# Performance work log

Measured on AMD Instinct MI355X. Metric: run time of the kernel, lower is better.

The kernel has to match this reference:

```python
import jax, jax.numpy as jnp
import numpy as np

NUM_HEADS = 32
HEAD_SIZE = 128
NUM_KV_HEADS = 8
SCALE = 0.08838834764831845  # 1/sqrt(128)
SLIDING_WINDOW = 1024
B, S = 2, 2048


def setup_inputs() -> dict:
    key = jax.random.key(0)
    kq, kk, kv = jax.random.split(key, 3)
    query = jax.random.normal(kq, (B, S, NUM_HEADS * HEAD_SIZE), dtype=jnp.float32)
    k = jax.random.normal(kk, (B, S, NUM_KV_HEADS * HEAD_SIZE), dtype=jnp.float32)
    v = jax.random.normal(kv, (B, S, NUM_KV_HEADS * HEAD_SIZE), dtype=jnp.float32)
    return {"query": query, "key": k, "value": v}


def _attn(query, key, value):
    # [B, S, H, D] / [B, S, KVH, D]
    q = query.reshape(B, S, NUM_HEADS, HEAD_SIZE)
    k = key.reshape(B, S, NUM_KV_HEADS, HEAD_SIZE)
    v = value.reshape(B, S, NUM_KV_HEADS, HEAD_SIZE)
    group = NUM_HEADS // NUM_KV_HEADS
    # GQA: broadcast each kv head across its query-head group
    k = jnp.repeat(k, group, axis=2)  # [B, S, H, D]
    v = jnp.repeat(v, group, axis=2)
    scores = jnp.einsum('bqhd,bkhd->bhqk', q, k) * SCALE  # [B, H, S, S]
    qi = jnp.arange(S)[:, None]
    ki = jnp.arange(S)[None, :]
    # causal + sliding window: key at most SLIDING_WINDOW-1 behind query
    mask = (ki <= qi) & (qi - ki < SLIDING_WINDOW)  # [S, S]
    neg_inf = jnp.finfo(scores.dtype).min
    scores = jnp.where(mask[None, None], scores, neg_inf)
    probs = jax.nn.softmax(scores, axis=-1)
    out = jnp.einsum('bhqk,bkhd->bqhd', probs, v)
    return out.reshape(B, S, NUM_HEADS * HEAD_SIZE)


def reference(query, key, value):
    return _attn(query, key, value)
```

## Files before the change

kernel.cpp:

```cpp
#include <hip/hip_runtime.h>
#include <hip/hip_bf16.h>


#define H_Q 32
#define H_KV 8
#define HDIM 128
#define SEQLEN 2048
#define NBATCH 2
#define WIN 1024
#define QK_SCALE 0.08838834764831845f
#define LOG2E 1.4426950408889634f
#define SCALE_LOG2E (QK_SCALE * LOG2E)

#define NEG_BIG  (-3.0e38f)
#define NEG_CLMP (-1.0e30f)

#define QPITCH (H_Q * HDIM)
#define KPITCH (H_KV * HDIM)

typedef __attribute__((ext_vector_type(8))) short  short8;
typedef __attribute__((ext_vector_type(4))) short  short4v;
typedef __attribute__((ext_vector_type(4))) float  floatx4;

static __device__ __forceinline__ short bf16bits(float x) {
    return __builtin_bit_cast(short, __float2bfloat16(x));
}

#define TR_READ(dst, addr, OFFSTR) \
    asm volatile("ds_read_b64_tr_b16 %0, %1 offset:" OFFSTR : "=v"(dst) : "v"(addr))

#define CAT8(a, b) __builtin_shufflevector(a, b, 0, 1, 2, 3, 4, 5, 6, 7)

#define MFMA_BF16 __builtin_amdgcn_mfma_f32_16x16x32_bf16

__global__ __launch_bounds__(256, 2)
void fa_fwd(const float* __restrict__ Q,
            const float* __restrict__ K,
            const float* __restrict__ V,
            float* __restrict__ O)
{
    __shared__ __align__(16) short lds_k[64][136];
    __shared__ __align__(16) short lds_v[8][64][16];
    __shared__ __align__(16) short lds_pt[4][64][16];

    const int bi  = blockIdx.x;
    const int qt  = bi & 31;
    const int h   = (bi >> 5) & 31;
    const int b   = bi >> 10;
    const int kvh = h >> 2;
    const int q0  = qt << 6;

    const int tid  = threadIdx.x;
    const int wid  = tid >> 6;
    const int lane = tid & 63;
    const int ln16 = lane & 15;
    const int lg   = lane >> 4;

    const float* Qb = Q + (size_t)b * SEQLEN * QPITCH + (size_t)h * HDIM;
    const float* Kb = K + (size_t)b * SEQLEN * KPITCH + (size_t)kvh * HDIM;
    const float* Vb = V + (size_t)b * SEQLEN * KPITCH + (size_t)kvh * HDIM;
    float*       Ob = O + (size_t)b * SEQLEN * QPITCH + (size_t)h * HDIM;

    const uint32_t v_base  = (uint32_t)(uintptr_t)&lds_v[0][0][0]
                           + (uint32_t)(lg * 256 + ln16 * 8);
    const uint32_t pt_base = (uint32_t)(uintptr_t)&lds_pt[wid][0][0]
                           + (uint32_t)(lg * 256 + ln16 * 8);

    int kvlo = q0 - (WIN - 1);
    if (kvlo < 0) kvlo = 0;
    kvlo &= ~63;

    floatx4 pk[8], pv[8];
    auto issue_kv = [&](int kt) {
        #pragma unroll
        for (int i = 0; i < 8; ++i) {
            const int fi  = i * 256 + tid;
            const int key = fi >> 5;
            const int c4  = (fi & 31) * 4;
            const size_t grow = (size_t)(kt + key) * KPITCH + c4;
            pk[i] = *(const floatx4*)(Kb + grow);
            pv[i] = *(const floatx4*)(Vb + grow);
        }
    };
    issue_kv(kvlo);

    short8 qf[4];
    {
        const int qrow = q0 + wid * 16 + ln16;
        const float* qs = Qb + (size_t)qrow * QPITCH + lg * 8;
        #pragma unroll
        for (int kk = 0; kk < 4; ++kk) {
            floatx4 a = *(const floatx4*)(qs + kk * 32);
            floatx4 c = *(const floatx4*)(qs + kk * 32 + 4);
            short8 f;
            #pragma unroll
            for (int j = 0; j < 4; ++j) { f[j] = bf16bits(a[j]); f[4 + j] = bf16bits(c[j]); }
            qf[kk] = f;
        }
    }

    floatx4 oacc[8];
    #pragma unroll
    for (int i = 0; i < 8; ++i) oacc[i] = (floatx4){0.f, 0.f, 0.f, 0.f};
    float m_r[4], l_r[4];
    #pragma unroll
    for (int r = 0; r < 4; ++r) { m_r[r] = NEG_BIG; l_r[r] = 0.f; }

    for (int kk0 = kvlo; kk0 <= q0; kk0 += 64) {
        __syncthreads();
        #pragma unroll
        for (int i = 0; i < 8; ++i) {
            const int fi  = i * 256 + tid;
            const int key = fi >> 5;
            const int c4  = (fi & 31) * 4;
            short4v ksv, vsv;
            #pragma unroll
            for (int j = 0; j < 4; ++j) {
                ksv[j] = bf16bits(pk[i][j]);
                vsv[j] = bf16bits(pv[i][j]);
            }
            *(short4v*)&lds_k[key][c4] = ksv;
            *(short4v*)&lds_v[c4 >> 4][key][c4 & 15] = vsv;
        }
        __syncthreads();

        if (kk0 + 64 <= q0) issue_kv(kk0 + 64);

        float sc[4][4];
        #pragma unroll
        for (int nt = 0; nt < 4; ++nt) {
            floatx4 acc = (floatx4){0.f, 0.f, 0.f, 0.f};
            #pragma unroll
            for (int kk = 0; kk < 4; ++kk) {
                short8 kf = *(const short8*)&lds_k[nt * 16 + ln16][kk * 32 + lg * 8];
                acc = MFMA_BF16(qf[kk], kf, acc, 0, 0, 0);
            }
            #pragma unroll
            for (int r = 0; r < 4; ++r) sc[nt][r] = acc[r];
        }

        const bool full = (kk0 + 63 <= q0) && (kk0 >= q0 - 960);
        float pm[4];
        #pragma unroll
        for (int r = 0; r < 4; ++r) pm[r] = NEG_BIG;
        if (full) {
            #pragma unroll
            for (int nt = 0; nt < 4; ++nt)
                #pragma unroll
                for (int r = 0; r < 4; ++r) {
                    sc[nt][r] *= SCALE_LOG2E;
                    pm[r] = fmaxf(pm[r], sc[nt][r]);
                }
        } else {
            #pragma unroll
            for (int nt = 0; nt < 4; ++nt) {
                const int kcol = kk0 + nt * 16 + ln16;
                #pragma unroll
                for (int r = 0; r < 4; ++r) {
                    const int qrow = q0 + wid * 16 + lg * 4 + r;
                    const bool ok = (kcol <= qrow) && (qrow - kcol < WIN);
                    sc[nt][r] = ok ? sc[nt][r] * SCALE_LOG2E : NEG_BIG;
                    pm[r] = fmaxf(pm[r], sc[nt][r]);
                }
            }
        }
        #pragma unroll
        for (int r = 0; r < 4; ++r)
            #pragma unroll
            for (int off = 1; off < 16; off <<= 1)
                pm[r] = fmaxf(pm[r], __shfl_xor(pm[r], off, 16));

        float alpha[4], mne[4];
        #pragma unroll
        for (int r = 0; r < 4; ++r) {
            const float mn = fmaxf(m_r[r], pm[r]);
            const float me = fmaxf(mn, NEG_CLMP);
            alpha[r] = exp2f(m_r[r] - me);
            m_r[r] = mn;
            mne[r] = me;
        }

        float psum[4] = {0.f, 0.f, 0.f, 0.f};
        #pragma unroll
        for (int nt = 0; nt < 4; ++nt) {
            short4v pq;
            #pragma unroll
            for (int r = 0; r < 4; ++r) {
                const float p = exp2f(sc[nt][r] - mne[r]);
                psum[r] += p;
                pq[r] = bf16bits(p);
            }
            *(short4v*)&lds_pt[wid][nt * 16 + ln16][lg * 4] = pq;
        }
        #pragma unroll
        for (int r = 0; r < 4; ++r) {
            #pragma unroll
            for (int off = 1; off < 16; off <<= 1)
                psum[r] += __shfl_xor(psum[r], off, 16);
            l_r[r] = l_r[r] * alpha[r] + psum[r];
        }
        #pragma unroll
        for (int dt = 0; dt < 8; ++dt)
            #pragma unroll
            for (int r = 0; r < 4; ++r) oacc[dt][r] *= alpha[r];

        asm volatile("s_waitcnt lgkmcnt(0)" ::: "memory");
        __builtin_amdgcn_sched_barrier(0);

        #pragma unroll
        for (int ks = 0; ks < 2; ++ks) {
            const uint32_t pa = pt_base + (uint32_t)(ks * 1024);
            const uint32_t va = v_base  + (uint32_t)(ks * 1024);
            short4v p0, p1, w0a, w0b, w1a, w1b, w2a, w2b, w3a, w3b;
            TR_READ(p0,  pa, "0");     TR_READ(p1,  pa, "128");
            TR_READ(w0a, va, "0");     TR_READ(w0b, va, "128");
            TR_READ(w1a, va, "2048");  TR_READ(w1b, va, "2176");
            TR_READ(w2a, va, "4096");  TR_READ(w2b, va, "4224");
            TR_READ(w3a, va, "6144");  TR_READ(w3b, va, "6272");
            asm volatile("s_waitcnt lgkmcnt(0)" ::: "memory");
            __builtin_amdgcn_sched_barrier(0);
            const short8 pf = CAT8(p0, p1);
            oacc[0] = MFMA_BF16(pf, CAT8(w0a, w0b), oacc[0], 0, 0, 0);
            oacc[1] = MFMA_BF16(pf, CAT8(w1a, w1b), oacc[1], 0, 0, 0);
            oacc[2] = MFMA_BF16(pf, CAT8(w2a, w2b), oacc[2], 0, 0, 0);
            oacc[3] = MFMA_BF16(pf, CAT8(w3a, w3b), oacc[3], 0, 0, 0);
            short4v x0a, x0b, x1a, x1b, x2a, x2b, x3a, x3b;
            TR_READ(x0a, va, "8192");  TR_READ(x0b, va, "8320");
            TR_READ(x1a, va, "10240"); TR_READ(x1b, va, "10368");
            TR_READ(x2a, va, "12288"); TR_READ(x2b, va, "12416");
            TR_READ(x3a, va, "14336"); TR_READ(x3b, va, "14464");
            asm volatile("s_waitcnt lgkmcnt(0)" ::: "memory");
            __builtin_amdgcn_sched_barrier(0);
            oacc[4] = MFMA_BF16(pf, CAT8(x0a, x0b), oacc[4], 0, 0, 0);
            oacc[5] = MFMA_BF16(pf, CAT8(x1a, x1b), oacc[5], 0, 0, 0);
            oacc[6] = MFMA_BF16(pf, CAT8(x2a, x2b), oacc[6], 0, 0, 0);
            oacc[7] = MFMA_BF16(pf, CAT8(x3a, x3b), oacc[7], 0, 0, 0);
        }
    }

    #pragma unroll
    for (int r = 0; r < 4; ++r) {
        const float inv = 1.0f / l_r[r];
        const int qrow = q0 + wid * 16 + lg * 4 + r;
        float* dst = Ob + (size_t)qrow * QPITCH;
        #pragma unroll
        for (int dt = 0; dt < 8; ++dt)
            dst[dt * 16 + ln16] = oacc[dt][r] * inv;
    }
}

extern "C" void kernel_launch(void* const* d_in, const int* in_sizes, int n_in,
                              void* d_out, int out_size, void* d_ws, size_t ws_size,
                              hipStream_t stream) {
    const float* Q = (const float*)d_in[0];
    const float* K = (const float*)d_in[1];
    const float* V = (const float*)d_in[2];
    float* O = (float*)d_out;
    dim3 grid(NBATCH * H_Q * (SEQLEN / 64));
    fa_fwd<<<grid, 256, 0, stream>>>(Q, K, V, O);
}
```

Baseline: 341.2 us.

## Pre-convert K/V to bf16 tiled workspace and stage via direct global-to-LDS loads

```diff
diff --git a/kernel.cpp b/kernel.cpp
--- a/kernel.cpp
+++ b/kernel.cpp
@@ -18,6 +18,9 @@
 #define QPITCH (H_Q * HDIM)
 #define KPITCH (H_KV * HDIM)
 
+#define WS_ELEMS ((size_t)NBATCH * H_KV * SEQLEN * HDIM)
+#define WS_BYTES (2 * WS_ELEMS * sizeof(short))
+
 typedef __attribute__((ext_vector_type(8))) short  short8;
 typedef __attribute__((ext_vector_type(4))) short  short4v;
 typedef __attribute__((ext_vector_type(4))) float  floatx4;
@@ -30,21 +33,54 @@
     asm volatile("ds_read_b64_tr_b16 %0, %1 offset:" OFFSTR : "=v"(dst) : "v"(addr))
 
 #define CAT8(a, b) __builtin_shufflevector(a, b, 0, 1, 2, 3, 4, 5, 6, 7)
-
 #define MFMA_BF16 __builtin_amdgcn_mfma_f32_16x16x32_bf16
 
-__global__ __launch_bounds__(256, 2)
+#define GLOAD_LDS16(gp, loff)                                                   \
+    __builtin_amdgcn_global_load_lds(                                           \
+        (const __attribute__((address_space(1))) unsigned int*)(const void*)(gp), \
+        (__attribute__((address_space(3))) unsigned int*)(uintptr_t)(loff),     \
+        16, 0, 0)
+
+#define CVT_THREADS (WS_ELEMS / 4)
+#define CVT_BLOCKS  (CVT_THREADS / 256)
+
+__global__ __launch_bounds__(256)
+void cvt_kv(const float* __restrict__ K, const float* __restrict__ V,
+            short* __restrict__ wsK, short* __restrict__ wsV)
+{
+    const int idx = blockIdx.x * 256 + threadIdx.x;
+    if (idx >= (int)CVT_THREADS) return;
+    const int g   = idx & 31;
+    const int kvh = (idx >> 5) & 7;
+    const int s   = (idx >> 8) & 2047;
+    const int b   = idx >> 19;
+    const int d   = g * 4;
+
+    const size_t soff = ((size_t)(b * SEQLEN + s)) * KPITCH + kvh * HDIM + d;
+    floatx4 kk = *(const floatx4*)(K + soff);
+    floatx4 vv = *(const floatx4*)(V + soff);
+    short4v ks, vs;
+    #pragma unroll
+    for (int j = 0; j < 4; ++j) { ks[j] = bf16bits(kk[j]); vs[j] = bf16bits(vv[j]); }
+
+    const size_t tbase = (((size_t)(b * H_KV + kvh)) * 32 + (s >> 6)) * 8192;
+    *(short4v*)&wsK[tbase + (size_t)(s & 63) * 128 + (d ^ ((s & 7) << 3))] = ks;
+    *(short4v*)&wsV[tbase + (size_t)(d >> 4) * 1024 + (s & 63) * 16 + (d & 15)] = vs;
+}
+
+__global__ __launch_bounds__(256, 4)
 void fa_fwd(const float* __restrict__ Q,
-            const float* __restrict__ K,
-            const float* __restrict__ V,
+            const short* __restrict__ wsK,
+            const short* __restrict__ wsV,
             float* __restrict__ O)
 {
-    __shared__ __align__(16) short lds_k[64][136];
+    __shared__ __align__(16) short lds_k[64][128];
     __shared__ __align__(16) short lds_v[8][64][16];
     __shared__ __align__(16) short lds_pt[4][64][16];
 
-    const int bi  = blockIdx.x;
-    const int qt  = bi & 31;
+    int bi = blockIdx.x;
+    bi = (bi & 7) * 256 + (bi >> 3);
+    const int qt  = 31 - (bi & 31);
     const int h   = (bi >> 5) & 31;
     const int b   = bi >> 10;
     const int kvh = h >> 2;
@@ -55,14 +91,18 @@
     const int lane = tid & 63;
     const int ln16 = lane & 15;
     const int lg   = lane >> 4;
+    const int kxor = (ln16 & 7) << 3;
 
     const float* Qb = Q + (size_t)b * SEQLEN * QPITCH + (size_t)h * HDIM;
-    const float* Kb = K + (size_t)b * SEQLEN * KPITCH + (size_t)kvh * HDIM;
-    const float* Vb = V + (size_t)b * SEQLEN * KPITCH + (size_t)kvh * HDIM;
     float*       Ob = O + (size_t)b * SEQLEN * QPITCH + (size_t)h * HDIM;
-
-    const uint32_t v_base  = (uint32_t)(uintptr_t)&lds_v[0][0][0]
-                           + (uint32_t)(lg * 256 + ln16 * 8);
+    const char*  wsKh = (const char*)(wsK + ((size_t)(b * H_KV + kvh)) * (SEQLEN * HDIM));
+    const char*  wsVh = (const char*)(wsV + ((size_t)(b * H_KV + kvh)) * (SEQLEN * HDIM));
+
+    const uint32_t k_lds = (uint32_t)(uintptr_t)&lds_k[0][0];
+    const uint32_t v_lds = (uint32_t)(uintptr_t)&lds_v[0][0][0];
+    const uint32_t wave_off = (uint32_t)((tid & 0xC0) * 16);
+
+    const uint32_t v_base  = v_lds + (uint32_t)(lg * 256 + ln16 * 8);
     const uint32_t pt_base = (uint32_t)(uintptr_t)&lds_pt[wid][0][0]
                            + (uint32_t)(lg * 256 + ln16 * 8);
 
@@ -70,19 +110,21 @@
     if (kvlo < 0) kvlo = 0;
     kvlo &= ~63;
 
-    floatx4 pk[8], pv[8];
-    auto issue_kv = [&](int kt) {
-        #pragma unroll
-        for (int i = 0; i < 8; ++i) {
-            const int fi  = i * 256 + tid;
-            const int key = fi >> 5;
-            const int c4  = (fi & 31) * 4;
-            const size_t grow = (size_t)(kt + key) * KPITCH + c4;
-            pk[i] = *(const floatx4*)(Kb + grow);
-            pv[i] = *(const floatx4*)(Vb + grow);
-        }
+    auto stage_k = [&](int kt) {
+        const char* src = wsKh + (size_t)kt * 16384;
+        #pragma unroll
+        for (int i = 0; i < 4; ++i)
+            GLOAD_LDS16(src + i * 4096 + tid * 16, k_lds + i * 4096 + wave_off);
     };
-    issue_kv(kvlo);
+    auto stage_v = [&](int kt) {
+        const char* src = wsVh + (size_t)kt * 16384;
+        #pragma unroll
+        for (int i = 0; i < 4; ++i)
+            GLOAD_LDS16(src + i * 4096 + tid * 16, v_lds + i * 4096 + wave_off);
+    };
+
+    stage_k(kvlo >> 6);
+    stage_v(kvlo >> 6);
 
     short8 qf[4];
     {
@@ -107,24 +149,12 @@
     for (int r = 0; r < 4; ++r) { m_r[r] = NEG_BIG; l_r[r] = 0.f; }
 
     for (int kk0 = kvlo; kk0 <= q0; kk0 += 64) {
-        __syncthreads();
-        #pragma unroll
-        for (int i = 0; i < 8; ++i) {
-            const int fi  = i * 256 + tid;
-            const int key = fi >> 5;
-            const int c4  = (fi & 31) * 4;
-            short4v ksv, vsv;
-            #pragma unroll
-            for (int j = 0; j < 4; ++j) {
-                ksv[j] = bf16bits(pk[i][j]);
-                vsv[j] = bf16bits(pv[i][j]);
-            }
-            *(short4v*)&lds_k[key][c4] = ksv;
-            *(short4v*)&lds_v[c4 >> 4][key][c4 & 15] = vsv;
-        }
-        __syncthreads();
-
-        if (kk0 + 64 <= q0) issue_kv(kk0 + 64);
+        const bool has_next = (kk0 + 64 <= q0);
+        const int  ktn = (kk0 >> 6) + 1;
+
+        asm volatile("s_waitcnt vmcnt(4)" ::: "memory");
+        __builtin_amdgcn_s_barrier();
+        __builtin_amdgcn_sched_barrier(0);
 
         float sc[4][4];
         #pragma unroll
@@ -132,7 +162,7 @@
             floatx4 acc = (floatx4){0.f, 0.f, 0.f, 0.f};
             #pragma unroll
             for (int kk = 0; kk < 4; ++kk) {
-                short8 kf = *(const short8*)&lds_k[nt * 16 + ln16][kk * 32 + lg * 8];
+                short8 kf = *(const short8*)&lds_k[nt * 16 + ln16][(kk * 32 + lg * 8) ^ kxor];
                 acc = MFMA_BF16(qf[kk], kf, acc, 0, 0, 0);
             }
             #pragma unroll
@@ -205,6 +235,13 @@
             for (int r = 0; r < 4; ++r) oacc[dt][r] *= alpha[r];
 
         asm volatile("s_waitcnt lgkmcnt(0)" ::: "memory");
+        __builtin_amdgcn_s_barrier();
+        __builtin_amdgcn_sched_barrier(0);
+        if (has_next) stage_k(ktn);
+
+        if (has_next) { asm volatile("s_waitcnt vmcnt(4)" ::: "memory"); }
+        else          { asm volatile("s_waitcnt vmcnt(0)" ::: "memory"); }
+        __builtin_amdgcn_s_barrier();
         __builtin_amdgcn_sched_barrier(0);
 
         #pragma unroll
@@ -236,6 +273,226 @@
             oacc[6] = MFMA_BF16(pf, CAT8(x2a, x2b), oacc[6], 0, 0, 0);
             oacc[7] = MFMA_BF16(pf, CAT8(x3a, x3b), oacc[7], 0, 0, 0);
         }
+
+        asm volatile("s_waitcnt lgkmcnt(0)" ::: "memory");
+        __builtin_amdgcn_s_barrier();
+        __builtin_amdgcn_sched_barrier(0);
+        if (has_next) stage_v(ktn);
+    }
+
+    #pragma unroll
+    for (int r = 0; r < 4; ++r) {
+        const float inv = 1.0f / l_r[r];
+        const int qrow = q0 + wid * 16 + lg * 4 + r;
+        float* dst = Ob + (size_t)qrow * QPITCH;
+        #pragma unroll
+        for (int dt = 0; dt < 8; ++dt)
+            dst[dt * 16 + ln16] = oacc[dt][r] * inv;
+    }
+}
+
+__global__ __launch_bounds__(256, 2)
+void fa_fwd_legacy(const float* __restrict__ Q,
+                   const float* __restrict__ K,
+                   const float* __restrict__ V,
+                   float* __restrict__ O)
+{
+    __shared__ __align__(16) short lds_k[64][136];
+    __shared__ __align__(16) short lds_v[8][64][16];
+    __shared__ __align__(16) short lds_pt[4][64][16];
+
+    const int bi  = blockIdx.x;
+    const int qt  = bi & 31;
+    const int h   = (bi >> 5) & 31;
+    const int b   = bi >> 10;
+    const int kvh = h >> 2;
+    const int q0  = qt << 6;
+
+    const int tid  = threadIdx.x;
+    const int wid  = tid >> 6;
+    const int lane = tid & 63;
+    const int ln16 = lane & 15;
+    const int lg   = lane >> 4;
+
+    const float* Qb = Q + (size_t)b * SEQLEN * QPITCH + (size_t)h * HDIM;
+    const float* Kb = K + (size_t)b * SEQLEN * KPITCH + (size_t)kvh * HDIM;
+    const float* Vb = V + (size_t)b * SEQLEN * KPITCH + (size_t)kvh * HDIM;
+    float*       Ob = O + (size_t)b * SEQLEN * QPITCH + (size_t)h * HDIM;
+
+    const uint32_t v_base  = (uint32_t)(uintptr_t)&lds_v[0][0][0]
+                           + (uint32_t)(lg * 256 + ln16 * 8);
+    const uint32_t pt_base = (uint32_t)(uintptr_t)&lds_pt[wid][0][0]
+                           + (uint32_t)(lg * 256 + ln16 * 8);
+
+    int kvlo = q0 - (WIN - 1);
+    if (kvlo < 0) kvlo = 0;
+    kvlo &= ~63;
+
+    floatx4 pk[8], pv[8];
+    auto issue_kv = [&](int kt) {
+        #pragma unroll
+        for (int i = 0; i < 8; ++i) {
+            const int fi  = i * 256 + tid;
+            const int key = fi >> 5;
+            const int c4  = (fi & 31) * 4;
+            const size_t grow = (size_t)(kt + key) * KPITCH + c4;
+            pk[i] = *(const floatx4*)(Kb + grow);
+            pv[i] = *(const floatx4*)(Vb + grow);
+        }
+    };
+    issue_kv(kvlo);
+
+    short8 qf[4];
+    {
+        const int qrow = q0 + wid * 16 + ln16;
+        const float* qs = Qb + (size_t)qrow * QPITCH + lg * 8;
+        #pragma unroll
+        for (int kk = 0; kk < 4; ++kk) {
+            floatx4 a = *(const floatx4*)(qs + kk * 32);
+            floatx4 c = *(const floatx4*)(qs + kk * 32 + 4);
+            short8 f;
+            #pragma unroll
+            for (int j = 0; j < 4; ++j) { f[j] = bf16bits(a[j]); f[4 + j] = bf16bits(c[j]); }
+            qf[kk] = f;
+        }
+    }
+
+    floatx4 oacc[8];
+    #pragma unroll
+    for (int i = 0; i < 8; ++i) oacc[i] = (floatx4){0.f, 0.f, 0.f, 0.f};
+    float m_r[4], l_r[4];
+    #pragma unroll
+    for (int r = 0; r < 4; ++r) { m_r[r] = NEG_BIG; l_r[r] = 0.f; }
+
+    for (int kk0 = kvlo; kk0 <= q0; kk0 += 64) {
+        __syncthreads();
+        #pragma unroll
+        for (int i = 0; i < 8; ++i) {
+            const int fi  = i * 256 + tid;
+            const int key = fi >> 5;
+            const int c4  = (fi & 31) * 4;
+            short4v ksv, vsv;
+            #pragma unroll
+            for (int j = 0; j < 4; ++j) {
+                ksv[j] = bf16bits(pk[i][j]);
+                vsv[j] = bf16bits(pv[i][j]);
+            }
+            *(short4v*)&lds_k[key][c4] = ksv;
+            *(short4v*)&lds_v[c4 >> 4][key][c4 & 15] = vsv;
+        }
+        __syncthreads();
+        if (kk0 + 64 <= q0) issue_kv(kk0 + 64);
+
+        float sc[4][4];
+        #pragma unroll
+        for (int nt = 0; nt < 4; ++nt) {
+            floatx4 acc = (floatx4){0.f, 0.f, 0.f, 0.f};
+            #pragma unroll
+            for (int kk = 0; kk < 4; ++kk) {
+                short8 kf = *(const short8*)&lds_k[nt * 16 + ln16][kk * 32 + lg * 8];
+                acc = MFMA_BF16(qf[kk], kf, acc, 0, 0, 0);
+            }
+            #pragma unroll
+            for (int r = 0; r < 4; ++r) sc[nt][r] = acc[r];
+        }
+
+        const bool full = (kk0 + 63 <= q0) && (kk0 >= q0 - 960);
+        float pm[4];
+        #pragma unroll
+        for (int r = 0; r < 4; ++r) pm[r] = NEG_BIG;
+        if (full) {
+            #pragma unroll
+            for (int nt = 0; nt < 4; ++nt)
+                #pragma unroll
+                for (int r = 0; r < 4; ++r) {
+                    sc[nt][r] *= SCALE_LOG2E;
+                    pm[r] = fmaxf(pm[r], sc[nt][r]);
+                }
+        } else {
+            #pragma unroll
+            for (int nt = 0; nt < 4; ++nt) {
+                const int kcol = kk0 + nt * 16 + ln16;
+                #pragma unroll
+                for (int r = 0; r < 4; ++r) {
+                    const int qrow = q0 + wid * 16 + lg * 4 + r;
+                    const bool ok = (kcol <= qrow) && (qrow - kcol < WIN);
+                    sc[nt][r] = ok ? sc[nt][r] * SCALE_LOG2E : NEG_BIG;
+                    pm[r] = fmaxf(pm[r], sc[nt][r]);
+                }
+            }
+        }
+        #pragma unroll
+        for (int r = 0; r < 4; ++r)
+            #pragma unroll
+            for (int off = 1; off < 16; off <<= 1)
+                pm[r] = fmaxf(pm[r], __shfl_xor(pm[r], off, 16));
+
+        float alpha[4], mne[4];
+        #pragma unroll
+        for (int r = 0; r < 4; ++r) {
+            const float mn = fmaxf(m_r[r], pm[r]);
+            const float me = fmaxf(mn, NEG_CLMP);
+            alpha[r] = exp2f(m_r[r] - me);
+            m_r[r] = mn;
+            mne[r] = me;
+        }
+
+        float psum[4] = {0.f, 0.f, 0.f, 0.f};
+        #pragma unroll
+        for (int nt = 0; nt < 4; ++nt) {
+            short4v pq;
+            #pragma unroll
+            for (int r = 0; r < 4; ++r) {
+                const float p = exp2f(sc[nt][r] - mne[r]);
+                psum[r] += p;
+                pq[r] = bf16bits(p);
+            }
+            *(short4v*)&lds_pt[wid][nt * 16 + ln16][lg * 4] = pq;
+        }
+        #pragma unroll
+        for (int r = 0; r < 4; ++r) {
+            #pragma unroll
+            for (int off = 1; off < 16; off <<= 1)
+                psum[r] += __shfl_xor(psum[r], off, 16);
+            l_r[r] = l_r[r] * alpha[r] + psum[r];
+        }
+        #pragma unroll
+        for (int dt = 0; dt < 8; ++dt)
+            #pragma unroll
+            for (int r = 0; r < 4; ++r) oacc[dt][r] *= alpha[r];
+
+        asm volatile("s_waitcnt lgkmcnt(0)" ::: "memory");
+        __builtin_amdgcn_sched_barrier(0);
+
+        #pragma unroll
+        for (int ks = 0; ks < 2; ++ks) {
+            const uint32_t pa = pt_base + (uint32_t)(ks * 1024);
+            const uint32_t va = v_base  + (uint32_t)(ks * 1024);
+            short4v p0, p1, w0a, w0b, w1a, w1b, w2a, w2b, w3a, w3b;
+            TR_READ(p0,  pa, "0");     TR_READ(p1,  pa, "128");
+            TR_READ(w0a, va, "0");     TR_READ(w0b, va, "128");
+            TR_READ(w1a, va, "2048");  TR_READ(w1b, va, "2176");
+            TR_READ(w2a, va, "4096");  TR_READ(w2b, va, "4224");
+            TR_READ(w3a, va, "6144");  TR_READ(w3b, va, "6272");
+            asm volatile("s_waitcnt lgkmcnt(0)" ::: "memory");
+            __builtin_amdgcn_sched_barrier(0);
+            const short8 pf = CAT8(p0, p1);
+            oacc[0] = MFMA_BF16(pf, CAT8(w0a, w0b), oacc[0], 0, 0, 0);
+            oacc[1] = MFMA_BF16(pf, CAT8(w1a, w1b), oacc[1], 0, 0, 0);
+            oacc[2] = MFMA_BF16(pf, CAT8(w2a, w2b), oacc[2], 0, 0, 0);
+            oacc[3] = MFMA_BF16(pf, CAT8(w3a, w3b), oacc[3], 0, 0, 0);
+            short4v x0a, x0b, x1a, x1b, x2a, x2b, x3a, x3b;
+            TR_READ(x0a, va, "8192");  TR_READ(x0b, va, "8320");
+            TR_READ(x1a, va, "10240"); TR_READ(x1b, va, "10368");
+            TR_READ(x2a, va, "12288"); TR_READ(x2b, va, "12416");
+            TR_READ(x3a, va, "14336"); TR_READ(x3b, va, "14464");
+            asm volatile("s_waitcnt lgkmcnt(0)" ::: "memory");
+            __builtin_amdgcn_sched_barrier(0);
+            oacc[4] = MFMA_BF16(pf, CAT8(x0a, x0b), oacc[4], 0, 0, 0);
+            oacc[5] = MFMA_BF16(pf, CAT8(x1a, x1b), oacc[5], 0, 0, 0);
+            oacc[6] = MFMA_BF16(pf, CAT8(x2a, x2b), oacc[6], 0, 0, 0);
+            oacc[7] = MFMA_BF16(pf, CAT8(x3a, x3b), oacc[7], 0, 0, 0);
+        }
     }
 
     #pragma unroll
@@ -257,5 +514,13 @@
     const float* V = (const float*)d_in[2];
     float* O = (float*)d_out;
     dim3 grid(NBATCH * H_Q * (SEQLEN / 64));
-    fa_fwd<<<grid, 256, 0, stream>>>(Q, K, V, O);
+
+    if (ws_size >= WS_BYTES && d_ws != nullptr) {
+        short* wsK = (short*)d_ws;
+        short* wsV = wsK + WS_ELEMS;
+        cvt_kv<<<dim3((unsigned)CVT_BLOCKS), 256, 0, stream>>>(K, V, wsK, wsV);
+        fa_fwd<<<grid, 256, 0, stream>>>(Q, wsK, wsV, O);
+    } else {
+        fa_fwd_legacy<<<grid, 256, 0, stream>>>(Q, K, V, O);
+    }
 }
```

Result: faster. 292.1 us (-14.4%).
